# Performance work log

Hardware: AMD Instinct MI355X
Metric: run time of the kernel (lower is better)

Reference implementation:

```python
import jax, jax.numpy as jnp
import numpy as np

N_DST0 = 20000  # number of dst nodes of block0 == src nodes of block1


def _graph_conv(x, src, dst, n_dst, W, b):
    # DGL GraphConv with norm='both': D_in^{-1/2} A D_out^{-1/2} X W + b
    e_ones = jnp.ones(src.shape[0], dtype=x.dtype)
    deg_out = jax.ops.segment_sum(e_ones, src, num_segments=x.shape[0])
    deg_in = jax.ops.segment_sum(e_ones, dst, num_segments=n_dst)
    xs = x * jax.lax.rsqrt(jnp.maximum(deg_out, 1.0))[:, None]
    agg = jax.ops.segment_sum(xs[src], dst, num_segments=n_dst)  # [n_dst, F]
    agg = agg * jax.lax.rsqrt(jnp.maximum(deg_in, 1.0))[:, None]
    return agg @ W + b


def setup_inputs() -> dict:
    key = jax.random.key(0)
    ks = jax.random.split(key, 10)
    vocab, emb, hid, out = 50000, 128, 256, 16
    n_src0, n_dst0, n_dst1 = 50000, N_DST0, 5000
    e0, e1 = 300000, 75000
    return {
        "user_word": jax.random.randint(ks[0], (n_src0, 10, 5), 0, vocab),
        "labels": jax.random.randint(ks[1], (n_dst1,), 0, out),
        "src0": jax.random.randint(ks[2], (e0,), 0, n_src0),
        "dst0": jax.random.randint(ks[3], (e0,), 0, n_dst0),
        "src1": jax.random.randint(ks[4], (e1,), 0, n_dst0),
        "dst1": jax.random.randint(ks[5], (e1,), 0, n_dst1),
        "word_table": jax.random.normal(ks[6], (vocab, emb), jnp.float32),
        "W1": jax.random.normal(ks[7], (emb, hid), jnp.float32) * 0.05,
        "b1": jnp.zeros((hid,), jnp.float32),
        "W2": jax.random.normal(ks[8], (hid, out), jnp.float32) * 0.05,
        "b2": jnp.zeros((out,), jnp.float32),
    }


def reference(user_word, labels, src0, dst0, src1, dst1, word_table, W1, b1, W2, b2):
    n_dst1 = labels.shape[0]
    # embedding gather + mean over words (dim=2) then items (dim=1)
    wf = word_table[user_word]                    # [n_src0, n_items, n_words, emb]
    x = jnp.mean(jnp.mean(wf, axis=2), axis=1)    # [n_src0, emb]
    x = jax.nn.relu(_graph_conv(x, src0, dst0, N_DST0, W1, b1))
    x = jax.nn.relu(_graph_conv(x, src1, dst1, n_dst1, W2, b2))
    x = x[:n_dst1]
    return (x, labels)
```

## Files before the change

### kernel.cpp

```cpp
#include <hip/hip_runtime.h>

#define E0     300000
#define E1     75000
#define NSRC0  50000
#define NDST0  20000
#define NDST1  5000
#define EMB    128
#define HID    256
#define NOUT   16

#define NPB        40
#define TILE_SHIFT 12
#define NEMB_BLK   (NSRC0 / NPB)

#define X0S  32.0f
#define H1S  64.0f

typedef __attribute__((ext_vector_type(8))) short bf16x8;
typedef __attribute__((ext_vector_type(4))) float f32x4;
typedef __attribute__((ext_vector_type(2))) float f32x2;

__device__ __forceinline__ unsigned short f2bf(float f) {
    unsigned u = __float_as_uint(f);
    return (unsigned short)((u + 0x7FFFu + ((u >> 16) & 1u)) >> 16);
}
__device__ __forceinline__ unsigned pack2(float a, float b) {
    return (unsigned)f2bf(a) | ((unsigned)f2bf(b) << 16);
}
__device__ __forceinline__ unsigned pack4_fp8(float a0, float a1, float a2, float a3) {
    unsigned p = 0;
    p = __builtin_amdgcn_cvt_pk_fp8_f32(a0, a1, p, false);
    p = __builtin_amdgcn_cvt_pk_fp8_f32(a2, a3, p, true);
    return p;
}
__device__ __forceinline__ unsigned char f2fp8(float v) {
    unsigned p = __builtin_amdgcn_cvt_pk_fp8_f32(v, v, 0, false);
    return (unsigned char)(p & 0xFF);
}
#if __has_builtin(__builtin_amdgcn_cvt_pk_f32_fp8)
__device__ __forceinline__ f32x2 up_lo(unsigned v) { return __builtin_amdgcn_cvt_pk_f32_fp8(v, false); }
__device__ __forceinline__ f32x2 up_hi(unsigned v) { return __builtin_amdgcn_cvt_pk_f32_fp8(v, true); }
#else
__device__ __forceinline__ f32x2 up_lo(unsigned v) {
    f32x2 r; r.x = __builtin_amdgcn_cvt_f32_fp8(v, 0); r.y = __builtin_amdgcn_cvt_f32_fp8(v, 1); return r;
}
__device__ __forceinline__ f32x2 up_hi(unsigned v) {
    f32x2 r; r.x = __builtin_amdgcn_cvt_f32_fp8(v, 2); r.y = __builtin_amdgcn_cvt_f32_fp8(v, 3); return r;
}
#endif

__global__ void prep_kernel(const float* __restrict__ wt, unsigned char* __restrict__ wt8,
                            const float* __restrict__ W1, unsigned short* __restrict__ W1Tb,
                            const float* __restrict__ W2, unsigned short* __restrict__ W2Tb,
                            const int* __restrict__ src0, const int* __restrict__ dst0,
                            const int* __restrict__ src1, const int* __restrict__ dst1,
                            int* cnt0, int* cnt1, int* degO0, int* degO1) {
    int i = blockIdx.x * blockDim.x + threadIdx.x;
    if (i < NSRC0 * EMB / 8) {
        const float4* in = (const float4*)wt;
        float4 v0 = in[i * 2], v1 = in[i * 2 + 1];
        uint2 o;
        o.x = pack4_fp8(v0.x, v0.y, v0.z, v0.w);
        o.y = pack4_fp8(v1.x, v1.y, v1.z, v1.w);
        ((uint2*)wt8)[i] = o;
    }
    if (i < EMB * HID) {
        int n = i & 255, k = i >> 8;
        W1Tb[n * 128 + k] = f2bf(W1[i]);
    }
    if (i < HID * NOUT) {
        int n = i & 15, k = i >> 4;
        W2Tb[n * 256 + k] = f2bf(W2[i]);
    }
    if (i < E0) {
        atomicAdd(&cnt0[dst0[i]], 1);
        atomicAdd(&degO0[src0[i]], 1);
    }
    if (i < E1) {
        atomicAdd(&cnt1[dst1[i]], 1);
        atomicAdd(&degO1[src1[i]], 1);
    }
}

__device__ void scan_body(const int* __restrict__ cnt, int n,
                          int* __restrict__ off, int* __restrict__ cur) {
    __shared__ int sums[1024];
    int t = threadIdx.x;
    int chunk = (n + 1023) / 1024;
    int lo = t * chunk, hi = min(lo + chunk, n);
    int s = 0;
    for (int i = lo; i < hi; ++i) s += cnt[i];
    sums[t] = s;
    __syncthreads();
    for (int d = 1; d < 1024; d <<= 1) {
        int x = (t >= d) ? sums[t - d] : 0;
        __syncthreads();
        sums[t] += x;
        __syncthreads();
    }
    int run = (t == 0) ? 0 : sums[t - 1];
    for (int i = lo; i < hi; ++i) {
        off[i] = run; cur[i] = run;
        run += cnt[i];
    }
    if (t == 1023) off[n] = run;
}

__global__ void scan_kernel(const int* cnt0, int* off0, int* cur0,
                            const int* cnt1, int* off1, int* cur1) {
    if (blockIdx.x == 0) scan_body(cnt0, NDST0, off0, cur0);
    else                 scan_body(cnt1, NDST1, off1, cur1);
}

__global__ void embed_bucket_kernel(const int* __restrict__ user_word,
                                    const unsigned char* __restrict__ wt8,
                                    const int* __restrict__ degO0,
                                    unsigned char* __restrict__ x0f,
                                    const int* __restrict__ src0, const int* __restrict__ dst0,
                                    const int* __restrict__ src1, const int* __restrict__ dst1,
                                    int* cur0, int* cur1, int* esrc0, int* esrc1) {
    if (blockIdx.x & 1) {
        int i = (blockIdx.x >> 1) * 256 + threadIdx.x;
        if (i < E0) {
            int p = atomicAdd(&cur0[dst0[i]], 1);
            esrc0[p] = src0[i];
        }
        if (i < E1) {
            int p = atomicAdd(&cur1[dst1[i]], 1);
            esrc1[p] = src1[i];
        }
        return;
    }
    int eb = blockIdx.x >> 1;
    __shared__ int raw[NPB * 50];
    __shared__ unsigned short srt[NPB * 50];
    int t = threadIdx.x;
    {
        const int4* uw4 = (const int4*)(user_word + eb * NPB * 50);
        int4* raw4 = (int4*)raw;
        for (int j = t; j < NPB * 50 / 4; j += 256)
            raw4[j] = uw4[j];
    }
    __syncthreads();
    {
        int wv = t >> 6, j = t & 63;
        unsigned long long lmlt = (1ULL << j) - 1;
        for (int n = wv; n < NPB; n += 4) {
            int word = 0, b = 16;
            if (j < 50) { word = raw[n * 50 + j]; b = word >> TILE_SHIFT; }
            int pos = 0;
            #pragma unroll
            for (int bb = 0; bb < 13; ++bb) {
                unsigned long long m = __ballot(b == bb);
                if (bb < b)       pos += __popcll(m);
                else if (bb == b) pos += __popcll(m & lmlt);
            }
            if (j < 50) srt[n * 50 + pos] = (unsigned short)word;
        }
    }
    __syncthreads();
    int g = t >> 5, l = t & 31;
    const unsigned* wt4 = (const unsigned*)wt8;
    const unsigned short* id[5];
    #pragma unroll
    for (int k = 0; k < 5; ++k) id[k] = srt + (g + 8 * k) * 50;
    f32x2 a01[5], a23[5];
    #pragma unroll
    for (int k = 0; k < 5; ++k) { a01[k] = (f32x2){0.f, 0.f}; a23[k] = (f32x2){0.f, 0.f}; }
    int j = 0;
    for (; j + 2 < 50; j += 3) {
        unsigned v[5][3];
        #pragma unroll
        for (int k = 0; k < 5; ++k)
            #pragma unroll
            for (int u = 0; u < 3; ++u)
                v[k][u] = wt4[(int)id[k][j + u] * 32 + l];
        #pragma unroll
        for (int k = 0; k < 5; ++k)
            #pragma unroll
            for (int u = 0; u < 3; ++u) {
                a01[k] += up_lo(v[k][u]); a23[k] += up_hi(v[k][u]);
            }
    }
    {
        unsigned v[5][2];
        #pragma unroll
        for (int k = 0; k < 5; ++k)
            #pragma unroll
            for (int u = 0; u < 2; ++u)
                v[k][u] = wt4[(int)id[k][48 + u] * 32 + l];
        #pragma unroll
        for (int k = 0; k < 5; ++k)
            #pragma unroll
            for (int u = 0; u < 2; ++u) {
                a01[k] += up_lo(v[k][u]); a23[k] += up_hi(v[k][u]);
            }
    }
    #pragma unroll
    for (int k = 0; k < 5; ++k) {
        int node = eb * NPB + g + k * 8;
        float s = rsqrtf(fmaxf((float)degO0[node], 1.0f)) * (0.02f * X0S);
        ((unsigned*)x0f)[node * 32 + l] =
            pack4_fp8(a01[k].x * s, a01[k].y * s, a23[k].x * s, a23[k].y * s);
    }
}

__global__ void layer1_kernel(const int* __restrict__ off0, const int* __restrict__ esrc0,
                              const unsigned char* __restrict__ x0f,
                              const int* __restrict__ degO1,
                              const unsigned short* __restrict__ W1Tb,
                              const float* __restrict__ b1,
                              unsigned char* __restrict__ h1f) {
    __shared__ unsigned short A[16 * 136];
    __shared__ float s_out[16];
    int t = threadIdx.x;
    int row0 = blockIdx.x * 16;
    int w = t >> 6, lane = t & 63;
    int half = lane >> 5, l = lane & 31;
    if (t < 16) s_out[t] = rsqrtf(fmaxf((float)degO1[row0 + t], 1.0f)) * H1S;
    {
        int d = row0 + w;
        int lo = off0[d], hi = off0[d + 1];
        const unsigned* x4 = (const unsigned*)x0f;
        f32x2 a01a = {0.f, 0.f}, a23a = {0.f, 0.f};
        f32x2 a01b = {0.f, 0.f}, a23b = {0.f, 0.f};
        int j = lo + half;
        for (; j + 6 < hi; j += 8) {
            unsigned va = x4[esrc0[j] * 32 + l];
            unsigned vb = x4[esrc0[j + 2] * 32 + l];
            unsigned vc = x4[esrc0[j + 4] * 32 + l];
            unsigned vd = x4[esrc0[j + 6] * 32 + l];
            a01a += up_lo(va); a23a += up_hi(va);
            a01b += up_lo(vb); a23b += up_hi(vb);
            a01a += up_lo(vc); a23a += up_hi(vc);
            a01b += up_lo(vd); a23b += up_hi(vd);
        }
        for (; j + 2 < hi; j += 4) {
            unsigned va = x4[esrc0[j] * 32 + l];
            unsigned vb = x4[esrc0[j + 2] * 32 + l];
            a01a += up_lo(va); a23a += up_hi(va);
            a01b += up_lo(vb); a23b += up_hi(vb);
        }
        if (j < hi) {
            unsigned v = x4[esrc0[j] * 32 + l];
            a01a += up_lo(v); a23a += up_hi(v);
        }
        f32x2 a01 = a01a + a01b, a23 = a23a + a23b;
        a01.x += __shfl_down(a01.x, 32); a01.y += __shfl_down(a01.y, 32);
        a23.x += __shfl_down(a23.x, 32); a23.y += __shfl_down(a23.y, 32);
        if (half == 0) {
            float sc = rsqrtf(fmaxf((float)(hi - lo), 1.0f)) * (1.0f / X0S);
            uint2 o; o.x = pack2(a01.x * sc, a01.y * sc); o.y = pack2(a23.x * sc, a23.y * sc);
            *(uint2*)(A + w * 136 + l * 4) = o;
        }
    }
    __syncthreads();
    int m = lane & 15, quad = lane >> 4;
    bf16x8 afr[4];
    #pragma unroll
    for (int ks = 0; ks < 4; ++ks)
        afr[ks] = *(const bf16x8*)(A + m * 136 + quad * 8 + ks * 32);
    int gcol0 = w * 16;
    const unsigned short* bbase = W1Tb + (gcol0 + m) * 128 + quad * 8;
    f32x4 acc = {0.f, 0.f, 0.f, 0.f};
    #pragma unroll
    for (int ks = 0; ks < 4; ++ks) {
        bf16x8 bfr = *(const bf16x8*)(bbase + ks * 32);
        acc = __builtin_amdgcn_mfma_f32_16x16x32_bf16(afr[ks], bfr, acc, 0, 0, 0);
    }
    int gcol = gcol0 + m;
    float bb = b1[gcol];
    #pragma unroll
    for (int reg = 0; reg < 4; ++reg) {
        int row = quad * 4 + reg;
        h1f[(row0 + row) * 256 + gcol] = f2fp8(fmaxf(acc[reg] + bb, 0.f) * s_out[row]);
    }
}

__global__ void layer2_kernel(const int* __restrict__ off1, const int* __restrict__ esrc1,
                              const unsigned char* __restrict__ h1f,
                              const unsigned short* __restrict__ W2Tb,
                              const float* __restrict__ b2,
                              const int* __restrict__ labels,
                              float* __restrict__ out) {
    __shared__ unsigned short A[16 * 264];
    int t = threadIdx.x;
    int row0 = blockIdx.x * 16;
    int w = t >> 6, lane = t & 63;
    {
        int d = row0 + w;
        f32x2 a01 = {0.f, 0.f}, a23 = {0.f, 0.f};
        float sc = 0.f;
        if (d < NDST1) {
            int lo = off1[d], hi = off1[d + 1];
            const unsigned* h4 = (const unsigned*)h1f;
            int j = lo;
            for (; j + 3 < hi; j += 4) {
                unsigned v0 = h4[esrc1[j] * 64 + lane];
                unsigned v1 = h4[esrc1[j + 1] * 64 + lane];
                unsigned v2 = h4[esrc1[j + 2] * 64 + lane];
                unsigned v3 = h4[esrc1[j + 3] * 64 + lane];
                a01 += up_lo(v0) + up_lo(v1) + up_lo(v2) + up_lo(v3);
                a23 += up_hi(v0) + up_hi(v1) + up_hi(v2) + up_hi(v3);
            }
            for (; j < hi; ++j) {
                unsigned v = h4[esrc1[j] * 64 + lane];
                a01 += up_lo(v); a23 += up_hi(v);
            }
            sc = rsqrtf(fmaxf((float)(hi - lo), 1.0f)) * (1.0f / H1S);
        }
        uint2 o; o.x = pack2(a01.x * sc, a01.y * sc); o.y = pack2(a23.x * sc, a23.y * sc);
        *(uint2*)(A + w * 264 + lane * 4) = o;
    }
    __syncthreads();
    if (w == 0) {
        int m = lane & 15, quad = lane >> 4;
        const unsigned short* bbase = W2Tb + m * 256 + quad * 8;
        f32x4 acc = {0.f, 0.f, 0.f, 0.f};
        #pragma unroll
        for (int ks = 0; ks < 8; ++ks) {
            bf16x8 af = *(const bf16x8*)(A + m * 264 + quad * 8 + ks * 32);
            bf16x8 bf = *(const bf16x8*)(bbase + ks * 32);
            acc = __builtin_amdgcn_mfma_f32_16x16x32_bf16(af, bf, acc, 0, 0, 0);
        }
        float bb = b2[m];
        #pragma unroll
        for (int reg = 0; reg < 4; ++reg) {
            int row = row0 + quad * 4 + reg;
            if (row < NDST1)
                out[row * NOUT + m] = fmaxf(acc[reg] + bb, 0.f);
        }
        if (lane < 16 && row0 + lane < NDST1)
            out[NDST1 * NOUT + row0 + lane] = (float)labels[row0 + lane];
    }
}

extern "C" void kernel_launch(void* const* d_in, const int* in_sizes, int n_in,
                              void* d_out, int out_size, void* d_ws, size_t ws_size,
                              hipStream_t stream) {
    const int*   user_word  = (const int*)d_in[0];
    const int*   labels     = (const int*)d_in[1];
    const int*   src0       = (const int*)d_in[2];
    const int*   dst0       = (const int*)d_in[3];
    const int*   src1       = (const int*)d_in[4];
    const int*   dst1       = (const int*)d_in[5];
    const float* word_table = (const float*)d_in[6];
    const float* W1         = (const float*)d_in[7];
    const float* b1         = (const float*)d_in[8];
    const float* W2         = (const float*)d_in[9];
    const float* b2         = (const float*)d_in[10];

    int* iws = (int*)d_ws;
    int* cnt0  = iws;
    int* cnt1  = iws + 20000;
    int* degO0 = iws + 25000;
    int* degO1 = iws + 75000;
    int* off0  = iws + 95000;
    int* off1  = iws + 115001;
    int* cur0  = iws + 120002;
    int* cur1  = iws + 140002;
    int* esrc0 = iws + 145002;
    int* esrc1 = iws + 445002;
    unsigned char*  wt8  = (unsigned char*)(iws + 520004);
    unsigned char*  x0f  = (unsigned char*)(iws + 2120004);
    unsigned char*  h1f  = (unsigned char*)(iws + 3720004);
    unsigned short* W1Tb = (unsigned short*)(iws + 5000004);
    unsigned short* W2Tb = (unsigned short*)(iws + 5008196);

    hipMemsetAsync(iws, 0, 95000 * sizeof(int), stream);

    prep_kernel<<<(NSRC0 * EMB / 8 + 255) / 256, 256, 0, stream>>>(
        word_table, wt8, W1, W1Tb, W2, W2Tb,
        src0, dst0, src1, dst1, cnt0, cnt1, degO0, degO1);
    scan_kernel<<<2, 1024, 0, stream>>>(cnt0, off0, cur0, cnt1, off1, cur1);
    embed_bucket_kernel<<<NEMB_BLK * 2, 256, 0, stream>>>(
        user_word, wt8, degO0, x0f,
        src0, dst0, src1, dst1, cur0, cur1, esrc0, esrc1);
    layer1_kernel<<<NDST0 / 16, 1024, 0, stream>>>(off0, esrc0, x0f, degO1, W1Tb, b1, h1f);
    layer2_kernel<<<(NDST1 + 15) / 16, 1024, 0, stream>>>(off1, esrc1, h1f, W2Tb, b2,
                                                          labels, (float*)d_out);
}
```

Measured before the change: 255.0 us.

## Split fp8 word table into column halves and spread edge bucketing across embed blocks

The fp8 word table is stored as two 64-byte column halves, each in its own contiguous region. Each embedding block now handles one half for its 40 nodes, with two 16-lane subgroups accumulating alternate words and combined by a cross-lane shuffle. The intent is to shrink the per-block gather footprint so L2 reuse of each half-table improves, at the cost of reading user_word and sorting twice per node group. Edge bucketing work is folded into the first 150 threads of every block instead of using separate dedicated blocks, which adds that work onto the embedding blocks.

```diff
diff --git a/kernel.cpp b/kernel.cpp
--- a/kernel.cpp
+++ b/kernel.cpp
@@ -11,7 +11,9 @@
 
 #define NPB        40
 #define TILE_SHIFT 12
-#define NEMB_BLK   (NSRC0 / NPB)
+#define NEB2       2504
+#define E0S        120
+#define E1S        30
 
 #define X0S  32.0f
 #define H1S  64.0f
@@ -62,7 +64,8 @@
         uint2 o;
         o.x = pack4_fp8(v0.x, v0.y, v0.z, v0.w);
         o.y = pack4_fp8(v1.x, v1.y, v1.z, v1.w);
-        ((uint2*)wt8)[i] = o;
+        int row = i >> 4, q = i & 15;
+        ((uint2*)wt8)[(q >> 3) * 400000 + row * 8 + (q & 7)] = o;
     }
     if (i < EMB * HID) {
         int n = i & 255, k = i >> 8;
@@ -119,22 +122,20 @@
                                     const int* __restrict__ src0, const int* __restrict__ dst0,
                                     const int* __restrict__ src1, const int* __restrict__ dst1,
                                     int* cur0, int* cur1, int* esrc0, int* esrc1) {
-    if (blockIdx.x & 1) {
-        int i = (blockIdx.x >> 1) * 256 + threadIdx.x;
-        if (i < E0) {
-            int p = atomicAdd(&cur0[dst0[i]], 1);
-            esrc0[p] = src0[i];
-        }
-        if (i < E1) {
-            int p = atomicAdd(&cur1[dst1[i]], 1);
-            esrc1[p] = src1[i];
-        }
-        return;
-    }
-    int eb = blockIdx.x >> 1;
+    int bi = blockIdx.x;
+    int t = threadIdx.x;
+    if (t < E0S) {
+        int i = bi * E0S + t;
+        if (i < E0) { int p = atomicAdd(&cur0[dst0[i]], 1); esrc0[p] = src0[i]; }
+    } else if (t < E0S + E1S) {
+        int i = bi * E1S + (t - E0S);
+        if (i < E1) { int p = atomicAdd(&cur1[dst1[i]], 1); esrc1[p] = src1[i]; }
+    }
+    int eb = (bi >> 3) * 4 + (bi & 3);
+    int half = (bi >> 2) & 1;
+    if (eb >= NSRC0 / NPB) return;
     __shared__ int raw[NPB * 50];
     __shared__ unsigned short srt[NPB * 50];
-    int t = threadIdx.x;
     {
         const int4* uw4 = (const int4*)(user_word + eb * NPB * 50);
         int4* raw4 = (int4*)raw;
@@ -160,48 +161,49 @@
     }
     __syncthreads();
     int g = t >> 5, l = t & 31;
-    const unsigned* wt4 = (const unsigned*)wt8;
+    int sub = l >> 4, c = l & 15;
+    const unsigned* wtp = (const unsigned*)(wt8 + half * (NSRC0 * 64));
     const unsigned short* id[5];
     #pragma unroll
     for (int k = 0; k < 5; ++k) id[k] = srt + (g + 8 * k) * 50;
-    f32x2 a01[5], a23[5];
-    #pragma unroll
-    for (int k = 0; k < 5; ++k) { a01[k] = (f32x2){0.f, 0.f}; a23[k] = (f32x2){0.f, 0.f}; }
+    f32x2 alo[5], ahi[5];
+    #pragma unroll
+    for (int k = 0; k < 5; ++k) { alo[k] = (f32x2){0.f, 0.f}; ahi[k] = (f32x2){0.f, 0.f}; }
     int j = 0;
-    for (; j + 2 < 50; j += 3) {
+    for (; j + 5 < 50; j += 6) {
         unsigned v[5][3];
         #pragma unroll
         for (int k = 0; k < 5; ++k)
             #pragma unroll
-            for (int u = 0; u < 3; ++u)
-                v[k][u] = wt4[(int)id[k][j + u] * 32 + l];
+            for (int p = 0; p < 3; ++p)
+                v[k][p] = wtp[(int)id[k][j + 2 * p + sub] * 16 + c];
         #pragma unroll
         for (int k = 0; k < 5; ++k)
             #pragma unroll
-            for (int u = 0; u < 3; ++u) {
-                a01[k] += up_lo(v[k][u]); a23[k] += up_hi(v[k][u]);
+            for (int p = 0; p < 3; ++p) {
+                alo[k] += up_lo(v[k][p]); ahi[k] += up_hi(v[k][p]);
             }
     }
     {
-        unsigned v[5][2];
-        #pragma unroll
-        for (int k = 0; k < 5; ++k)
-            #pragma unroll
-            for (int u = 0; u < 2; ++u)
-                v[k][u] = wt4[(int)id[k][48 + u] * 32 + l];
-        #pragma unroll
-        for (int k = 0; k < 5; ++k)
-            #pragma unroll
-            for (int u = 0; u < 2; ++u) {
-                a01[k] += up_lo(v[k][u]); a23[k] += up_hi(v[k][u]);
-            }
+        unsigned v[5];
+        #pragma unroll
+        for (int k = 0; k < 5; ++k) v[k] = wtp[(int)id[k][48 + sub] * 16 + c];
+        #pragma unroll
+        for (int k = 0; k < 5; ++k) { alo[k] += up_lo(v[k]); ahi[k] += up_hi(v[k]); }
     }
     #pragma unroll
     for (int k = 0; k < 5; ++k) {
-        int node = eb * NPB + g + k * 8;
-        float s = rsqrtf(fmaxf((float)degO0[node], 1.0f)) * (0.02f * X0S);
-        ((unsigned*)x0f)[node * 32 + l] =
-            pack4_fp8(a01[k].x * s, a01[k].y * s, a23[k].x * s, a23[k].y * s);
+        alo[k].x += __shfl_xor(alo[k].x, 16); alo[k].y += __shfl_xor(alo[k].y, 16);
+        ahi[k].x += __shfl_xor(ahi[k].x, 16); ahi[k].y += __shfl_xor(ahi[k].y, 16);
+    }
+    if (sub == 0) {
+        #pragma unroll
+        for (int k = 0; k < 5; ++k) {
+            int node = eb * NPB + g + 8 * k;
+            float s = rsqrtf(fmaxf((float)degO0[node], 1.0f)) * (0.02f * X0S);
+            ((unsigned*)x0f)[node * 32 + half * 16 + c] =
+                pack4_fp8(alo[k].x * s, alo[k].y * s, ahi[k].x * s, ahi[k].y * s);
+        }
     }
 }
 
@@ -373,7 +375,7 @@
         word_table, wt8, W1, W1Tb, W2, W2Tb,
         src0, dst0, src1, dst1, cnt0, cnt1, degO0, degO1);
     scan_kernel<<<2, 1024, 0, stream>>>(cnt0, off0, cur0, cnt1, off1, cur1);
-    embed_bucket_kernel<<<NEMB_BLK * 2, 256, 0, stream>>>(
+    embed_bucket_kernel<<<NEB2, 256, 0, stream>>>(
         user_word, wt8, degO0, x0f,
         src0, dst0, src1, dst1, cur0, cur1, esrc0, esrc1);
     layer1_kernel<<<NDST0 / 16, 1024, 0, stream>>>(off0, esrc0, x0f, degO1, W1Tb, b1, h1f);
```

New measurement: 247.9 us (median of 2 runs). 1.03x faster.
